# Optimization experiments

Measured on AMD Instinct MI355X. Metric: run time of the kernel, lower is better.

The kernel has to match this reference:

```python
import jax, jax.numpy as jnp
import numpy as np

N_THETA = 180
N_PHI = 360
LOSS_WEIGHT = 1.0
SIGMA = 1.0


def _gaussian_kernel():
    x = jnp.arange(N_THETA, dtype=jnp.float32)
    y = jnp.arange(N_PHI, dtype=jnp.float32)
    xx, yy = jnp.meshgrid(x, y, indexing='ij')
    k = jnp.exp(-((xx - N_THETA // 2) ** 2 + (yy - N_PHI // 2) ** 2) / (2 * SIGMA ** 2))
    return k / k.sum()


def _vector_to_bins(vec):
    theta = jnp.arccos(jnp.clip(vec[:, 2], -1.0, 1.0))
    phi = jnp.arctan2(vec[:, 1], vec[:, 0])
    phi = jnp.where(phi < 0, phi + 2 * jnp.pi, phi)
    theta_idx = jnp.clip((theta / jnp.pi * N_THETA).astype(jnp.int32), 0, N_THETA - 1)
    phi_idx = jnp.clip((phi / (2 * jnp.pi) * N_PHI).astype(jnp.int32), 0, N_PHI - 1)
    return theta_idx, phi_idx


def _smooth_labels(theta_idx, phi_idx, kernel):
    # Shifted gaussian centered at (theta_idx, phi_idx), zero outside kernel extent, renormalized.
    si = jnp.arange(N_THETA)[None, :] - theta_idx[:, None] + N_THETA // 2  # [B, T]
    sj = jnp.arange(N_PHI)[None, :] - phi_idx[:, None] + N_PHI // 2      # [B, P]
    mi = (si >= 0) & (si < N_THETA)
    mj = (sj >= 0) & (sj < N_PHI)
    lab = kernel[jnp.clip(si, 0, N_THETA - 1)[:, :, None],
                 jnp.clip(sj, 0, N_PHI - 1)[:, None, :]]  # [B, T, P]
    lab = lab * (mi[:, :, None] & mj[:, None, :]).astype(kernel.dtype)
    return lab / lab.sum(axis=(1, 2), keepdims=True)


def _bce(p, y):
    # torch F.binary_cross_entropy clamps log terms at -100
    lp = jnp.clip(jnp.log(p), -100.0)
    lq = jnp.clip(jnp.log1p(-p), -100.0)
    return jnp.mean(-(y * lp + (1.0 - y) * lq))


def setup_inputs() -> dict:
    key = jax.random.key(0)
    k1, k2, k3 = jax.random.split(key, 3)
    B = 1024
    eps = 1e-4
    probs = jax.random.uniform(k1, (B, 2, N_THETA, N_PHI), dtype=jnp.float32,
                               minval=eps, maxval=1.0 - eps)
    gt_u = jax.random.normal(k2, (B, 3), dtype=jnp.float32)
    gt_u = gt_u / jnp.linalg.norm(gt_u, axis=1, keepdims=True)
    gt_r = jax.random.normal(k3, (B, 3), dtype=jnp.float32)
    gt_r = gt_r / jnp.linalg.norm(gt_r, axis=1, keepdims=True)
    return {"probs": probs, "gt_u": gt_u, "gt_r": gt_r}


def reference(probs, gt_u, gt_r):
    kernel = _gaussian_kernel()
    probs_u, probs_r = probs[:, 0], probs[:, 1]
    tu, pu = _vector_to_bins(gt_u)
    tr, pr = _vector_to_bins(gt_r)
    labels_u = _smooth_labels(tu, pu, kernel)
    labels_r = _smooth_labels(tr, pr, kernel)
    loss = _bce(probs_u, labels_u) + _bce(probs_r, labels_r)
    return loss * LOSS_WEIGHT
```

## Files before the change

kernel.cpp:

```cpp
#include <hip/hip_runtime.h>

#define NTH 180
#define NPH 360
#define BATCH 1024

#define LOG2_CLIP (-144.26950408889634f)
#define LN2F 0.6931471805599453f

__global__ void zero_acc_kernel(double* acc) {
    if (threadIdx.x == 0) { acc[0] = 0.0; acc[1] = 0.0; }
}

__global__ __launch_bounds__(256) void dense_sum_kernel(
    const float* __restrict__ probs, long long n4, double* __restrict__ acc) {
    const float4* __restrict__ p4 = (const float4*)probs;
    long long idx = (long long)blockIdx.x * blockDim.x + threadIdx.x;
    long long stride = (long long)gridDim.x * blockDim.x;
    float s = 0.0f;
    for (long long i = idx; i < n4; i += stride) {
        float4 v = p4[i];
        s += fmaxf(__log2f(1.0f - v.x), LOG2_CLIP);
        s += fmaxf(__log2f(1.0f - v.y), LOG2_CLIP);
        s += fmaxf(__log2f(1.0f - v.z), LOG2_CLIP);
        s += fmaxf(__log2f(1.0f - v.w), LOG2_CLIP);
    }
    #pragma unroll
    for (int off = 32; off > 0; off >>= 1) s += __shfl_down(s, off);
    __shared__ float wsum[4];
    int lane = threadIdx.x & 63, wid = threadIdx.x >> 6;
    if (lane == 0) wsum[wid] = s;
    __syncthreads();
    if (threadIdx.x == 0) {
        float bs = wsum[0] + wsum[1] + wsum[2] + wsum[3];
        unsafeAtomicAdd(acc, (double)(-LN2F * bs));
    }
}

__global__ __launch_bounds__(64) void label_term_kernel(
    const float* __restrict__ probs, const float* __restrict__ gt_u,
    const float* __restrict__ gt_r, double* __restrict__ acc) {
    int bc = blockIdx.x;
    int b = bc >> 1;
    int c = bc & 1;
    const float* g = (c == 0) ? gt_u : gt_r;
    float gx = g[b * 3 + 0], gy = g[b * 3 + 1], gz = g[b * 3 + 2];

    float theta = acosf(fminf(fmaxf(gz, -1.0f), 1.0f));
    float phi = atan2f(gy, gx);
    if (phi < 0.0f) phi += 6.283185307179586f;
    int t = (int)(theta / 3.14159265358979323846f * (float)NTH);
    t = min(max(t, 0), NTH - 1);
    int pb = (int)(phi / 6.283185307179586f * (float)NPH);
    pb = min(max(pb, 0), NPH - 1);

    const int R = 12;
    int i0 = max(0, t - R), i1 = min(NTH - 1, t + R);
    int j0 = max(0, pb - R), j1 = min(NPH - 1, pb + R);

    float zt = 0.0f, zp = 0.0f;
    for (int i = i0; i <= i1; ++i) { float d = (float)(i - t);  zt += __expf(-0.5f * d * d); }
    for (int j = j0; j <= j1; ++j) { float d = (float)(j - pb); zp += __expf(-0.5f * d * d); }
    float invZ = 1.0f / (zt * zp);

    const float* __restrict__ P = probs + ((long long)b * 2 + c) * (NTH * NPH);
    int nj = j1 - j0 + 1;
    int npts = (i1 - i0 + 1) * nj;
    float s = 0.0f;
    for (int k = threadIdx.x; k < npts; k += 64) {
        int i = i0 + k / nj;
        int j = j0 + k % nj;
        float di = (float)(i - t), dj = (float)(j - pb);
        float w = __expf(-0.5f * (di * di + dj * dj));
        float pv = P[i * NPH + j];
        float lp = fmaxf(__logf(pv), -100.0f);
        float lq = fmaxf(__logf(1.0f - pv), -100.0f);
        s += w * (lq - lp);
    }
    #pragma unroll
    for (int off = 32; off > 0; off >>= 1) s += __shfl_down(s, off);
    if (threadIdx.x == 0) unsafeAtomicAdd(acc + 1, (double)(s * invZ));
}

__global__ void finalize_kernel(const double* __restrict__ acc, float* __restrict__ out) {
    if (threadIdx.x == 0) {
        double denom = (double)BATCH * (double)NTH * (double)NPH;
        out[0] = (float)((acc[0] + acc[1]) / denom);
    }
}

extern "C" void kernel_launch(void* const* d_in, const int* in_sizes, int n_in,
                              void* d_out, int out_size, void* d_ws, size_t ws_size,
                              hipStream_t stream) {
    const float* probs = (const float*)d_in[0];
    const float* gt_u  = (const float*)d_in[1];
    const float* gt_r  = (const float*)d_in[2];
    float* out = (float*)d_out;
    double* acc = (double*)d_ws;

    long long n = (long long)in_sizes[0];
    long long n4 = n / 4;

    zero_acc_kernel<<<1, 64, 0, stream>>>(acc);
    dense_sum_kernel<<<2048, 256, 0, stream>>>(probs, n4, acc);
    label_term_kernel<<<2048, 64, 0, stream>>>(probs, gt_u, gt_r, acc);
    finalize_kernel<<<1, 64, 0, stream>>>(acc, out);
}
```

Measured before the change: 700.6 us.

## Fuse dense sum and label term kernels, replace atomics with partial reduction

Merges the dense log(1-p) pass and the per-sample label window pass into one kernel with 2048 blocks of 256 threads, hardcoding the trip count and tail of the dense loop for the fixed input size. Per-block partial sums go to a workspace buffer and a single-block kernel reduces them, replacing the double atomics and the zero and finalize launches. This removes two launches and the atomic traffic, and the label work now uses 256 threads per block instead of 64. In exchange the kernel is tied to the fixed batch size, and the label window reads now sit behind the dense loop within each block.

```diff
diff --git a/kernel.cpp b/kernel.cpp
--- a/kernel.cpp
+++ b/kernel.cpp
@@ -3,54 +3,51 @@
 #define NTH 180
 #define NPH 360
 #define BATCH 1024
+#define NBLK 2048
+#define NTHREADS 256
 
 #define LOG2_CLIP (-144.26950408889634f)
 #define LN2F 0.6931471805599453f
 
-__global__ void zero_acc_kernel(double* acc) {
-    if (threadIdx.x == 0) { acc[0] = 0.0; acc[1] = 0.0; }
-}
+#define N4_MAIN_ITERS 63
+#define N4_TAIL_BASE 33030144
+#define N4_TAIL 147456
 
-__global__ __launch_bounds__(256) void dense_sum_kernel(
-    const float* __restrict__ probs, long long n4, double* __restrict__ acc) {
+__global__ __launch_bounds__(NTHREADS) void fused_kernel(
+    const float* __restrict__ probs, const float* __restrict__ gt_u,
+    const float* __restrict__ gt_r, float2* __restrict__ partial) {
     const float4* __restrict__ p4 = (const float4*)probs;
-    long long idx = (long long)blockIdx.x * blockDim.x + threadIdx.x;
-    long long stride = (long long)gridDim.x * blockDim.x;
-    float s = 0.0f;
-    for (long long i = idx; i < n4; i += stride) {
-        float4 v = p4[i];
-        s += fmaxf(__log2f(1.0f - v.x), LOG2_CLIP);
-        s += fmaxf(__log2f(1.0f - v.y), LOG2_CLIP);
-        s += fmaxf(__log2f(1.0f - v.z), LOG2_CLIP);
-        s += fmaxf(__log2f(1.0f - v.w), LOG2_CLIP);
+    int idx = blockIdx.x * NTHREADS + threadIdx.x;
+    const int stride = NBLK * NTHREADS;
+
+    float sd = 0.0f;
+    #pragma unroll 4
+    for (int it = 0; it < N4_MAIN_ITERS; ++it) {
+        float4 v = p4[idx + it * stride];
+        sd += fmaxf(__log2f(1.0f - v.x), LOG2_CLIP);
+        sd += fmaxf(__log2f(1.0f - v.y), LOG2_CLIP);
+        sd += fmaxf(__log2f(1.0f - v.z), LOG2_CLIP);
+        sd += fmaxf(__log2f(1.0f - v.w), LOG2_CLIP);
     }
-    #pragma unroll
-    for (int off = 32; off > 0; off >>= 1) s += __shfl_down(s, off);
-    __shared__ float wsum[4];
-    int lane = threadIdx.x & 63, wid = threadIdx.x >> 6;
-    if (lane == 0) wsum[wid] = s;
-    __syncthreads();
-    if (threadIdx.x == 0) {
-        float bs = wsum[0] + wsum[1] + wsum[2] + wsum[3];
-        unsafeAtomicAdd(acc, (double)(-LN2F * bs));
+    if (idx < N4_TAIL) {
+        float4 v = p4[N4_TAIL_BASE + idx];
+        sd += fmaxf(__log2f(1.0f - v.x), LOG2_CLIP);
+        sd += fmaxf(__log2f(1.0f - v.y), LOG2_CLIP);
+        sd += fmaxf(__log2f(1.0f - v.z), LOG2_CLIP);
+        sd += fmaxf(__log2f(1.0f - v.w), LOG2_CLIP);
     }
-}
 
-__global__ __launch_bounds__(64) void label_term_kernel(
-    const float* __restrict__ probs, const float* __restrict__ gt_u,
-    const float* __restrict__ gt_r, double* __restrict__ acc) {
-    int bc = blockIdx.x;
-    int b = bc >> 1;
-    int c = bc & 1;
+    int b = blockIdx.x >> 1;
+    int c = blockIdx.x & 1;
     const float* g = (c == 0) ? gt_u : gt_r;
     float gx = g[b * 3 + 0], gy = g[b * 3 + 1], gz = g[b * 3 + 2];
 
     float theta = acosf(fminf(fmaxf(gz, -1.0f), 1.0f));
     float phi = atan2f(gy, gx);
     if (phi < 0.0f) phi += 6.283185307179586f;
-    int t = (int)(theta / 3.14159265358979323846f * (float)NTH);
+    int t = (int)(theta * (1.0f / 3.14159265358979323846f) * (float)NTH);
     t = min(max(t, 0), NTH - 1);
-    int pb = (int)(phi / 6.283185307179586f * (float)NPH);
+    int pb = (int)(phi * (1.0f / 6.283185307179586f) * (float)NPH);
     pb = min(max(pb, 0), NPH - 1);
 
     const int R = 12;
@@ -62,11 +59,11 @@
     for (int j = j0; j <= j1; ++j) { float d = (float)(j - pb); zp += __expf(-0.5f * d * d); }
     float invZ = 1.0f / (zt * zp);
 
-    const float* __restrict__ P = probs + ((long long)b * 2 + c) * (NTH * NPH);
+    const float* __restrict__ P = probs + (blockIdx.x * (NTH * NPH));
     int nj = j1 - j0 + 1;
     int npts = (i1 - i0 + 1) * nj;
-    float s = 0.0f;
-    for (int k = threadIdx.x; k < npts; k += 64) {
+    float sl = 0.0f;
+    for (int k = threadIdx.x; k < npts; k += NTHREADS) {
         int i = i0 + k / nj;
         int j = j0 + k % nj;
         float di = (float)(i - t), dj = (float)(j - pb);
@@ -74,17 +71,42 @@
         float pv = P[i * NPH + j];
         float lp = fmaxf(__logf(pv), -100.0f);
         float lq = fmaxf(__logf(1.0f - pv), -100.0f);
-        s += w * (lq - lp);
+        sl += w * (lq - lp);
+    }
+
+    #pragma unroll
+    for (int off = 32; off > 0; off >>= 1) {
+        sd += __shfl_down(sd, off);
+        sl += __shfl_down(sl, off);
+    }
+    __shared__ float wsd[4], wsl[4];
+    int lane = threadIdx.x & 63, wid = threadIdx.x >> 6;
+    if (lane == 0) { wsd[wid] = sd; wsl[wid] = sl; }
+    __syncthreads();
+    if (threadIdx.x == 0) {
+        float bd = wsd[0] + wsd[1] + wsd[2] + wsd[3];
+        float bl = wsl[0] + wsl[1] + wsl[2] + wsl[3];
+        partial[blockIdx.x] = make_float2(-LN2F * bd, invZ * bl);
+    }
+}
+
+__global__ __launch_bounds__(NTHREADS) void reduce_kernel(
+    const float2* __restrict__ partial, float* __restrict__ out) {
+    double s = 0.0;
+    for (int i = threadIdx.x; i < NBLK; i += NTHREADS) {
+        float2 v = partial[i];
+        s += (double)v.x + (double)v.y;
     }
     #pragma unroll
     for (int off = 32; off > 0; off >>= 1) s += __shfl_down(s, off);
-    if (threadIdx.x == 0) unsafeAtomicAdd(acc + 1, (double)(s * invZ));
-}
-
-__global__ void finalize_kernel(const double* __restrict__ acc, float* __restrict__ out) {
+    __shared__ double wsum[4];
+    int lane = threadIdx.x & 63, wid = threadIdx.x >> 6;
+    if (lane == 0) wsum[wid] = s;
+    __syncthreads();
     if (threadIdx.x == 0) {
+        double tot = wsum[0] + wsum[1] + wsum[2] + wsum[3];
         double denom = (double)BATCH * (double)NTH * (double)NPH;
-        out[0] = (float)((acc[0] + acc[1]) / denom);
+        out[0] = (float)(tot / denom);
     }
 }
 
@@ -95,13 +117,8 @@
     const float* gt_u  = (const float*)d_in[1];
     const float* gt_r  = (const float*)d_in[2];
     float* out = (float*)d_out;
-    double* acc = (double*)d_ws;
+    float2* partial = (float2*)d_ws;
 
-    long long n = (long long)in_sizes[0];
-    long long n4 = n / 4;
-
-    zero_acc_kernel<<<1, 64, 0, stream>>>(acc);
-    dense_sum_kernel<<<2048, 256, 0, stream>>>(probs, n4, acc);
-    label_term_kernel<<<2048, 64, 0, stream>>>(probs, gt_u, gt_r, acc);
-    finalize_kernel<<<1, 64, 0, stream>>>(acc, out);
+    fused_kernel<<<NBLK, NTHREADS, 0, stream>>>(probs, gt_u, gt_r, partial);
+    reduce_kernel<<<1, NTHREADS, 0, stream>>>(partial, out);
 }
```

New measurement: 674.8 us. 1.04x faster.
